# Kernel tuning notes

Measured on AMD Instinct MI355X. Metric: run time of the kernel, lower is better.

The kernel has to match this reference:

```python
import jax, jax.numpy as jnp
import numpy as np

EPS = 1e-3
MAX_ITER = 100
STAB = 1e-8


def setup_inputs() -> dict:
    key = jax.random.key(0)
    k1, k2 = jax.random.split(key)
    x = jax.random.normal(k1, (4, 4096, 8, 8), dtype=jnp.float32)
    y = jax.random.normal(k2, (4, 4096, 8, 8), dtype=jnp.float32)
    return {"x": x, "y": y}


def _sinkhorn_distance(x, y):
    B, N, H, W = x.shape
    d = H * W
    xf = jax.nn.softmax(x.reshape(B, N, d), axis=-1)  # [B,N,d]
    yf = jax.nn.softmax(y.reshape(B, N, d), axis=-1)  # [B,N,d]

    # squared euclidean distance: ||a-b||^2 = ||a||^2 + ||b||^2 - 2 a.b  (== cdist(p=2)**2)
    x2 = jnp.sum(xf * xf, axis=-1)  # [B,N]
    y2 = jnp.sum(yf * yf, axis=-1)  # [B,N]
    cross = jnp.einsum('bid,bjd->bij', xf, yf)  # [B,N,N]
    cost = jnp.maximum(x2[:, :, None] + y2[:, None, :] - 2.0 * cross, 0.0)

    K = jnp.exp(-cost / EPS)  # [B,N,N]

    u0 = jnp.full((B, N), 1.0 / N, dtype=x.dtype)
    v0 = jnp.full((B, N), 1.0 / N, dtype=x.dtype)

    def step(carry, _):
        u, v = carry
        u = 1.0 / (jnp.einsum('bij,bj->bi', K, v) + STAB)
        v = 1.0 / (jnp.einsum('bij,bi->bj', K, u) + STAB)
        return (u, v), None

    (u, v), _ = jax.lax.scan(step, (u0, v0), None, length=MAX_ITER)

    plan = u[:, :, None] * K * v[:, None, :]  # [B,N,N]
    dist = jnp.sum(plan * cost, axis=(1, 2))  # [B]
    return jnp.sum(dist)  # reduction='sum'


def reference(x, y):
    return _sinkhorn_distance(x, y)
```

## Files before the change

kernel.cpp:

```cpp
#include <hip/hip_runtime.h>
#include <stdint.h>

#define BB 4
#define NN 4096
#define DD 64
#define BN (BB*NN)
#define STABF 1e-8f
#define NITER 100
#define NEG_SCALE (-1442.695040888963f)

__device__ __forceinline__ float bf16lo(uint32_t w){ return __uint_as_float(w << 16); }
__device__ __forceinline__ float bf16hi(uint32_t w){ return __uint_as_float(w & 0xffff0000u); }
__device__ __forceinline__ uint32_t pack2bf(float f0, float f1){
  uint32_t u0 = __float_as_uint(f0); u0 += 0x7fffu + ((u0 >> 16) & 1u);
  uint32_t u1 = __float_as_uint(f1); u1 += 0x7fffu + ((u1 >> 16) & 1u);
  return (u0 >> 16) | (u1 & 0xffff0000u);
}

__global__ __launch_bounds__(256) void k_init(float* __restrict__ acc0,
                                              float* __restrict__ partial) {
  int idx = blockIdx.x * 256 + threadIdx.x;
  if (idx < BN) acc0[idx] = (float)NN;
  if (idx < 256) partial[idx] = 0.f;
}

__global__ __launch_bounds__(256) void k_softmax(
    const float* __restrict__ x, const float* __restrict__ y,
    float* __restrict__ xf, float* __restrict__ yf,
    float* __restrict__ x2, float* __restrict__ y2) {
  int wave = (blockIdx.x * 256 + threadIdx.x) >> 6;
  int lane = threadIdx.x & 63;
  const float* src; float* dst; float* d2; int row;
  if (wave < BN) { src = x; dst = xf; d2 = x2; row = wave; }
  else           { src = y; dst = yf; d2 = y2; row = wave - BN; }
  float v = src[(size_t)row * DD + lane];
  float m = v;
  #pragma unroll
  for (int off = 32; off; off >>= 1) m = fmaxf(m, __shfl_xor(m, off));
  float e = __expf(v - m);
  float s = e;
  #pragma unroll
  for (int off = 32; off; off >>= 1) s += __shfl_xor(s, off);
  float p = e / s;
  dst[(size_t)row * DD + lane] = p;
  float q = p * p;
  #pragma unroll
  for (int off = 32; off; off >>= 1) q += __shfl_xor(q, off);
  if (lane == 0) d2[row] = q;
}

__device__ __forceinline__ void fma_row(float av0, float av1, const float4 bv,
                                        float cr0[4], float cr1[4]) {
  cr0[0] = fmaf(av0, bv.x, cr0[0]); cr0[1] = fmaf(av0, bv.y, cr0[1]);
  cr0[2] = fmaf(av0, bv.z, cr0[2]); cr0[3] = fmaf(av0, bv.w, cr0[3]);
  cr1[0] = fmaf(av1, bv.x, cr1[0]); cr1[1] = fmaf(av1, bv.y, cr1[1]);
  cr1[2] = fmaf(av1, bv.z, cr1[2]); cr1[3] = fmaf(av1, bv.w, cr1[3]);
}

__global__ __launch_bounds__(256) void k_build(
    const float* __restrict__ xf, const float* __restrict__ yf,
    const float* __restrict__ x2, const float* __restrict__ y2,
    unsigned short* __restrict__ K) {
  __shared__ float sxf[32][68];
  __shared__ float syt[64][68];
  int bid = blockIdx.x, t = threadIdx.x;
  int jt = bid & 63, it = (bid >> 6) & 127, b = bid >> 13;
  int i0 = it * 32, j0 = jt * 64;
  {
    int r = t >> 3, c = (t & 7) * 8;
    const float* s0 = xf + ((size_t)(b*NN + i0 + r)) * DD + c;
    *(float4*)&sxf[r][c]     = *(const float4*)s0;
    *(float4*)&sxf[r][c + 4] = *(const float4*)(s0 + 4);
  }
  {
    int r = t >> 2, c0 = (t & 3) * 16;
    const float* s0 = yf + ((size_t)(b*NN + j0 + r)) * DD + c0;
    #pragma unroll
    for (int q = 0; q < 4; ++q) {
      float4 pv = *(const float4*)(s0 + q*4);
      syt[c0 + q*4 + 0][r] = pv.x;
      syt[c0 + q*4 + 1][r] = pv.y;
      syt[c0 + q*4 + 2][r] = pv.z;
      syt[c0 + q*4 + 3][r] = pv.w;
    }
  }
  __syncthreads();
  int tx = t & 15, ty = t >> 4;
  int ii = ty * 2, jj = tx * 4;
  float cr[2][4] = {{0,0,0,0},{0,0,0,0}};
  #pragma unroll
  for (int d = 0; d < DD; d += 4) {
    float4 a0 = *(const float4*)&sxf[ii][d];
    float4 a1 = *(const float4*)&sxf[ii + 1][d];
    float4 b0 = *(const float4*)&syt[d][jj];
    float4 b1 = *(const float4*)&syt[d + 1][jj];
    float4 b2 = *(const float4*)&syt[d + 2][jj];
    float4 b3 = *(const float4*)&syt[d + 3][jj];
    fma_row(a0.x, a1.x, b0, cr[0], cr[1]);
    fma_row(a0.y, a1.y, b1, cr[0], cr[1]);
    fma_row(a0.z, a1.z, b2, cr[0], cr[1]);
    fma_row(a0.w, a1.w, b3, cr[0], cr[1]);
  }
  float x2v[2], y2v[4];
  x2v[0] = x2[b*NN + i0 + ii]; x2v[1] = x2[b*NN + i0 + ii + 1];
  #pragma unroll
  for (int c = 0; c < 4; ++c) y2v[c] = y2[b*NN + j0 + jj + c];
  #pragma unroll
  for (int i2 = 0; i2 < 2; ++i2) {
    float k4[4];
    #pragma unroll
    for (int c = 0; c < 4; ++c) {
      float cost = fmaxf(x2v[i2] + y2v[c] - 2.f * cr[i2][c], 0.f);
      k4[c] = exp2f(cost * NEG_SCALE);
    }
    uint2 kw;
    kw.x = pack2bf(k4[0], k4[1]);
    kw.y = pack2bf(k4[2], k4[3]);
    *(uint2*)(K + ((size_t)(b*NN + i0 + ii + i2)) * NN + j0 + jj) = kw;
  }
}

__global__ __launch_bounds__(256) void k_rowdot(
    const unsigned short* __restrict__ K, const float* __restrict__ accIn,
    float* __restrict__ u, float* __restrict__ accZ) {
  int bid = blockIdx.x, t = threadIdx.x;
  if (bid < 16) {
    float4 z = make_float4(0.f, 0.f, 0.f, 0.f);
    *(float4*)(accZ + (size_t)(bid * 256 + t) * 4) = z;
  }
  int b = bid >> 8, g = bid & 255;
  int wave = t >> 6, lane = t & 63;
  const float* ap = accIn + (size_t)b * NN + lane * 8;
  float4 vr[16];
  #pragma unroll
  for (int c = 0; c < 8; ++c) {
    vr[2*c]   = *(const float4*)(ap + c * 512);
    vr[2*c+1] = *(const float4*)(ap + c * 512 + 4);
  }
  #pragma unroll
  for (int c = 0; c < 16; ++c) {
    vr[c].x = __builtin_amdgcn_rcpf(vr[c].x + STABF);
    vr[c].y = __builtin_amdgcn_rcpf(vr[c].y + STABF);
    vr[c].z = __builtin_amdgcn_rcpf(vr[c].z + STABF);
    vr[c].w = __builtin_amdgcn_rcpf(vr[c].w + STABF);
  }
  int row0 = g * 16 + wave * 4;
  const unsigned short* Kp = K + ((size_t)(b*NN + row0)) * NN + lane * 8;
  float s0 = 0.f, s1 = 0.f, s2 = 0.f, s3 = 0.f;
  #pragma unroll
  for (int c = 0; c < 8; ++c) {
    uint4 k0 = *(const uint4*)(Kp + (size_t)0 * NN + c * 512);
    uint4 k1 = *(const uint4*)(Kp + (size_t)1 * NN + c * 512);
    uint4 k2 = *(const uint4*)(Kp + (size_t)2 * NN + c * 512);
    uint4 k3 = *(const uint4*)(Kp + (size_t)3 * NN + c * 512);
    float4 a0 = vr[2*c], a1 = vr[2*c+1];
    s0 = fmaf(bf16lo(k0.x), a0.x, s0); s0 = fmaf(bf16hi(k0.x), a0.y, s0);
    s0 = fmaf(bf16lo(k0.y), a0.z, s0); s0 = fmaf(bf16hi(k0.y), a0.w, s0);
    s0 = fmaf(bf16lo(k0.z), a1.x, s0); s0 = fmaf(bf16hi(k0.z), a1.y, s0);
    s0 = fmaf(bf16lo(k0.w), a1.z, s0); s0 = fmaf(bf16hi(k0.w), a1.w, s0);
    s1 = fmaf(bf16lo(k1.x), a0.x, s1); s1 = fmaf(bf16hi(k1.x), a0.y, s1);
    s1 = fmaf(bf16lo(k1.y), a0.z, s1); s1 = fmaf(bf16hi(k1.y), a0.w, s1);
    s1 = fmaf(bf16lo(k1.z), a1.x, s1); s1 = fmaf(bf16hi(k1.z), a1.y, s1);
    s1 = fmaf(bf16lo(k1.w), a1.z, s1); s1 = fmaf(bf16hi(k1.w), a1.w, s1);
    s2 = fmaf(bf16lo(k2.x), a0.x, s2); s2 = fmaf(bf16hi(k2.x), a0.y, s2);
    s2 = fmaf(bf16lo(k2.y), a0.z, s2); s2 = fmaf(bf16hi(k2.y), a0.w, s2);
    s2 = fmaf(bf16lo(k2.z), a1.x, s2); s2 = fmaf(bf16hi(k2.z), a1.y, s2);
    s2 = fmaf(bf16lo(k2.w), a1.z, s2); s2 = fmaf(bf16hi(k2.w), a1.w, s2);
    s3 = fmaf(bf16lo(k3.x), a0.x, s3); s3 = fmaf(bf16hi(k3.x), a0.y, s3);
    s3 = fmaf(bf16lo(k3.y), a0.z, s3); s3 = fmaf(bf16hi(k3.y), a0.w, s3);
    s3 = fmaf(bf16lo(k3.z), a1.x, s3); s3 = fmaf(bf16hi(k3.z), a1.y, s3);
    s3 = fmaf(bf16lo(k3.w), a1.z, s3); s3 = fmaf(bf16hi(k3.w), a1.w, s3);
  }
  #pragma unroll
  for (int off = 32; off; off >>= 1) {
    s0 += __shfl_xor(s0, off);
    s1 += __shfl_xor(s1, off);
    s2 += __shfl_xor(s2, off);
    s3 += __shfl_xor(s3, off);
  }
  if (lane == 0) {
    float* up = u + b*NN + row0;
    up[0] = 1.0f / (s0 + STABF);
    up[1] = 1.0f / (s1 + STABF);
    up[2] = 1.0f / (s2 + STABF);
    up[3] = 1.0f / (s3 + STABF);
  }
}

__global__ __launch_bounds__(256) void k_coldot(
    const unsigned short* __restrict__ K, const float* __restrict__ u,
    float* __restrict__ acc) {
  int bid = blockIdx.x, t = threadIdx.x;
  int slab = bid & 1, chunk = (bid >> 1) & 63, b = bid >> 7;
  int i0 = chunk * 64;
  int j0 = slab * 2048 + t * 8;
  const unsigned short* Kp = K + ((size_t)(b*NN + i0)) * NN + j0;
  const float* up = u + b*NN + i0;
  float s0=0,s1=0,s2=0,s3=0,s4=0,s5=0,s6=0,s7=0;
  #pragma unroll 4
  for (int r = 0; r < 64; ++r) {
    uint4 kw = *(const uint4*)(Kp + (size_t)r * NN);
    float ur = up[r];
    s0 = fmaf(bf16lo(kw.x), ur, s0);
    s1 = fmaf(bf16hi(kw.x), ur, s1);
    s2 = fmaf(bf16lo(kw.y), ur, s2);
    s3 = fmaf(bf16hi(kw.y), ur, s3);
    s4 = fmaf(bf16lo(kw.z), ur, s4);
    s5 = fmaf(bf16hi(kw.z), ur, s5);
    s6 = fmaf(bf16lo(kw.w), ur, s6);
    s7 = fmaf(bf16hi(kw.w), ur, s7);
  }
  float* ap = acc + b*NN + j0;
  atomicAdd(ap + 0, s0); atomicAdd(ap + 1, s1);
  atomicAdd(ap + 2, s2); atomicAdd(ap + 3, s3);
  atomicAdd(ap + 4, s4); atomicAdd(ap + 5, s5);
  atomicAdd(ap + 6, s6); atomicAdd(ap + 7, s7);
}

__global__ __launch_bounds__(256) void k_final(
    const float* __restrict__ xf, const float* __restrict__ yf,
    const float* __restrict__ x2, const float* __restrict__ y2,
    const unsigned short* __restrict__ K, const float* __restrict__ u,
    const float* __restrict__ accv, float* __restrict__ partial) {
  __shared__ float sxf[32][68];
  __shared__ float syt[64][68];
  __shared__ float red[256];
  int bid = blockIdx.x, t = threadIdx.x;
  int jt = bid & 63, it = (bid >> 6) & 127, b = bid >> 13;
  int i0 = it * 32, j0 = jt * 64;
  {
    int r = t >> 3, c = (t & 7) * 8;
    const float* s0 = xf + ((size_t)(b*NN + i0 + r)) * DD + c;
    *(float4*)&sxf[r][c]     = *(const float4*)s0;
    *(float4*)&sxf[r][c + 4] = *(const float4*)(s0 + 4);
  }
  {
    int r = t >> 2, c0 = (t & 3) * 16;
    const float* s0 = yf + ((size_t)(b*NN + j0 + r)) * DD + c0;
    #pragma unroll
    for (int q = 0; q < 4; ++q) {
      float4 pv = *(const float4*)(s0 + q*4);
      syt[c0 + q*4 + 0][r] = pv.x;
      syt[c0 + q*4 + 1][r] = pv.y;
      syt[c0 + q*4 + 2][r] = pv.z;
      syt[c0 + q*4 + 3][r] = pv.w;
    }
  }
  __syncthreads();
  int tx = t & 15, ty = t >> 4;
  int ii = ty * 2, jj = tx * 4;
  float cr[2][4] = {{0,0,0,0},{0,0,0,0}};
  #pragma unroll
  for (int d = 0; d < DD; d += 4) {
    float4 a0 = *(const float4*)&sxf[ii][d];
    float4 a1 = *(const float4*)&sxf[ii + 1][d];
    float4 b0 = *(const float4*)&syt[d][jj];
    float4 b1 = *(const float4*)&syt[d + 1][jj];
    float4 b2 = *(const float4*)&syt[d + 2][jj];
    float4 b3 = *(const float4*)&syt[d + 3][jj];
    fma_row(a0.x, a1.x, b0, cr[0], cr[1]);
    fma_row(a0.y, a1.y, b1, cr[0], cr[1]);
    fma_row(a0.z, a1.z, b2, cr[0], cr[1]);
    fma_row(a0.w, a1.w, b3, cr[0], cr[1]);
  }
  float x2v[2], y2v[4], uv[2], vv[4];
  x2v[0] = x2[b*NN + i0 + ii]; x2v[1] = x2[b*NN + i0 + ii + 1];
  uv[0]  = u[b*NN + i0 + ii];  uv[1]  = u[b*NN + i0 + ii + 1];
  #pragma unroll
  for (int c = 0; c < 4; ++c) {
    y2v[c] = y2[b*NN + j0 + jj + c];
    vv[c]  = __builtin_amdgcn_rcpf(accv[b*NN + j0 + jj + c] + STABF);
  }
  float s = 0.f;
  #pragma unroll
  for (int i2 = 0; i2 < 2; ++i2) {
    uint2 kw = *(const uint2*)(K + ((size_t)(b*NN + i0 + ii + i2)) * NN + j0 + jj);
    float kk[4] = {bf16lo(kw.x), bf16hi(kw.x), bf16lo(kw.y), bf16hi(kw.y)};
    #pragma unroll
    for (int c = 0; c < 4; ++c) {
      float cost = fmaxf(x2v[i2] + y2v[c] - 2.f * cr[i2][c], 0.f);
      s = fmaf(uv[i2] * kk[c] * vv[c], cost, s);
    }
  }
  red[t] = s;
  __syncthreads();
  #pragma unroll
  for (int off = 128; off; off >>= 1) {
    if (t < off) red[t] += red[t + off];
    __syncthreads();
  }
  if (t == 0) atomicAdd(partial + (bid & 255), red[0]);
}

__global__ __launch_bounds__(256) void k_finalize(const float* __restrict__ partial,
                                                 float* __restrict__ out) {
  __shared__ float red[256];
  int t = threadIdx.x;
  red[t] = partial[t];
  __syncthreads();
  #pragma unroll
  for (int off = 128; off; off >>= 1) {
    if (t < off) red[t] += red[t + off];
    __syncthreads();
  }
  if (t == 0) out[0] = red[0];
}

extern "C" void kernel_launch(void* const* d_in, const int* in_sizes, int n_in,
                              void* d_out, int out_size, void* d_ws, size_t ws_size,
                              hipStream_t stream) {
  const float* x = (const float*)d_in[0];
  const float* y = (const float*)d_in[1];
  float* out = (float*)d_out;

  char* w = (char*)d_ws;
  unsigned short* K = (unsigned short*)w;
  float* xf = (float*)(w + (size_t)BN * NN * 2);
  float* yf = xf + (size_t)BN * DD;
  float* x2 = yf + (size_t)BN * DD;
  float* y2 = x2 + BN;
  float* uu = y2 + BN;
  float* acc = uu + BN;
  float* partial = acc + 2 * BN;
  (void)in_sizes; (void)n_in; (void)out_size; (void)ws_size;

  k_init<<<64, 256, 0, stream>>>(acc, partial);
  k_softmax<<<8192, 256, 0, stream>>>(x, y, xf, yf, x2, y2);
  k_build<<<32768, 256, 0, stream>>>(xf, yf, x2, y2, K);

  int p = 0;
  for (int itr = 0; itr < NITER; ++itr) {
    k_rowdot<<<1024, 256, 0, stream>>>(K, acc + (size_t)p * BN, uu, acc + (size_t)(1 - p) * BN);
    k_coldot<<<512, 256, 0, stream>>>(K, uu, acc + (size_t)(1 - p) * BN);
    p ^= 1;
  }
  k_final<<<32768, 256, 0, stream>>>(xf, yf, x2, y2, K, uu, acc, partial);
  k_finalize<<<1, 256, 0, stream>>>(partial, out);
}
```

Baseline: 7.698 ms.

## Fuse Sinkhorn row and column passes into one kernel with triple-buffered accumulators

```diff
diff --git a/kernel.cpp b/kernel.cpp
--- a/kernel.cpp
+++ b/kernel.cpp
@@ -18,9 +18,10 @@
 }
 
 __global__ __launch_bounds__(256) void k_init(float* __restrict__ acc0,
+                                              float* __restrict__ acc1,
                                               float* __restrict__ partial) {
   int idx = blockIdx.x * 256 + threadIdx.x;
-  if (idx < BN) acc0[idx] = (float)NN;
+  if (idx < BN) { acc0[idx] = (float)NN; acc1[idx] = 0.f; }
   if (idx < 256) partial[idx] = 0.f;
 }
 
@@ -120,101 +121,124 @@
   }
 }
 
-__global__ __launch_bounds__(256) void k_rowdot(
+__global__ __launch_bounds__(256, 2) void k_step(
     const unsigned short* __restrict__ K, const float* __restrict__ accIn,
-    float* __restrict__ u, float* __restrict__ accZ) {
+    float* __restrict__ accOut, float* __restrict__ accZero,
+    float* __restrict__ u) {
   int bid = blockIdx.x, t = threadIdx.x;
   if (bid < 16) {
     float4 z = make_float4(0.f, 0.f, 0.f, 0.f);
-    *(float4*)(accZ + (size_t)(bid * 256 + t) * 4) = z;
-  }
-  int b = bid >> 8, g = bid & 255;
+    *(float4*)(accZero + (size_t)(bid * 256 + t) * 4) = z;
+  }
+  int b = bid >> 7, chunk = bid & 127;
+  int i0 = chunk * 32;
   int wave = t >> 6, lane = t & 63;
-  const float* ap = accIn + (size_t)b * NN + lane * 8;
-  float4 vr[16];
-  #pragma unroll
-  for (int c = 0; c < 8; ++c) {
-    vr[2*c]   = *(const float4*)(ap + c * 512);
-    vr[2*c+1] = *(const float4*)(ap + c * 512 + 4);
-  }
-  #pragma unroll
-  for (int c = 0; c < 16; ++c) {
-    vr[c].x = __builtin_amdgcn_rcpf(vr[c].x + STABF);
-    vr[c].y = __builtin_amdgcn_rcpf(vr[c].y + STABF);
-    vr[c].z = __builtin_amdgcn_rcpf(vr[c].z + STABF);
-    vr[c].w = __builtin_amdgcn_rcpf(vr[c].w + STABF);
-  }
-  int row0 = g * 16 + wave * 4;
-  const unsigned short* Kp = K + ((size_t)(b*NN + row0)) * NN + lane * 8;
-  float s0 = 0.f, s1 = 0.f, s2 = 0.f, s3 = 0.f;
-  #pragma unroll
-  for (int c = 0; c < 8; ++c) {
-    uint4 k0 = *(const uint4*)(Kp + (size_t)0 * NN + c * 512);
-    uint4 k1 = *(const uint4*)(Kp + (size_t)1 * NN + c * 512);
-    uint4 k2 = *(const uint4*)(Kp + (size_t)2 * NN + c * 512);
-    uint4 k3 = *(const uint4*)(Kp + (size_t)3 * NN + c * 512);
-    float4 a0 = vr[2*c], a1 = vr[2*c+1];
-    s0 = fmaf(bf16lo(k0.x), a0.x, s0); s0 = fmaf(bf16hi(k0.x), a0.y, s0);
-    s0 = fmaf(bf16lo(k0.y), a0.z, s0); s0 = fmaf(bf16hi(k0.y), a0.w, s0);
-    s0 = fmaf(bf16lo(k0.z), a1.x, s0); s0 = fmaf(bf16hi(k0.z), a1.y, s0);
-    s0 = fmaf(bf16lo(k0.w), a1.z, s0); s0 = fmaf(bf16hi(k0.w), a1.w, s0);
-    s1 = fmaf(bf16lo(k1.x), a0.x, s1); s1 = fmaf(bf16hi(k1.x), a0.y, s1);
-    s1 = fmaf(bf16lo(k1.y), a0.z, s1); s1 = fmaf(bf16hi(k1.y), a0.w, s1);
-    s1 = fmaf(bf16lo(k1.z), a1.x, s1); s1 = fmaf(bf16hi(k1.z), a1.y, s1);
-    s1 = fmaf(bf16lo(k1.w), a1.z, s1); s1 = fmaf(bf16hi(k1.w), a1.w, s1);
-    s2 = fmaf(bf16lo(k2.x), a0.x, s2); s2 = fmaf(bf16hi(k2.x), a0.y, s2);
-    s2 = fmaf(bf16lo(k2.y), a0.z, s2); s2 = fmaf(bf16hi(k2.y), a0.w, s2);
-    s2 = fmaf(bf16lo(k2.z), a1.x, s2); s2 = fmaf(bf16hi(k2.z), a1.y, s2);
-    s2 = fmaf(bf16lo(k2.w), a1.z, s2); s2 = fmaf(bf16hi(k2.w), a1.w, s2);
-    s3 = fmaf(bf16lo(k3.x), a0.x, s3); s3 = fmaf(bf16hi(k3.x), a0.y, s3);
-    s3 = fmaf(bf16lo(k3.y), a0.z, s3); s3 = fmaf(bf16hi(k3.y), a0.w, s3);
-    s3 = fmaf(bf16lo(k3.z), a1.x, s3); s3 = fmaf(bf16hi(k3.z), a1.y, s3);
-    s3 = fmaf(bf16lo(k3.w), a1.z, s3); s3 = fmaf(bf16hi(k3.w), a1.w, s3);
-  }
-  #pragma unroll
-  for (int off = 32; off; off >>= 1) {
-    s0 += __shfl_xor(s0, off);
-    s1 += __shfl_xor(s1, off);
-    s2 += __shfl_xor(s2, off);
-    s3 += __shfl_xor(s3, off);
-  }
-  if (lane == 0) {
-    float* up = u + b*NN + row0;
-    up[0] = 1.0f / (s0 + STABF);
-    up[1] = 1.0f / (s1 + STABF);
-    up[2] = 1.0f / (s2 + STABF);
-    up[3] = 1.0f / (s3 + STABF);
-  }
-}
-
-__global__ __launch_bounds__(256) void k_coldot(
-    const unsigned short* __restrict__ K, const float* __restrict__ u,
-    float* __restrict__ acc) {
-  int bid = blockIdx.x, t = threadIdx.x;
-  int slab = bid & 1, chunk = (bid >> 1) & 63, b = bid >> 7;
-  int i0 = chunk * 64;
-  int j0 = slab * 2048 + t * 8;
-  const unsigned short* Kp = K + ((size_t)(b*NN + i0)) * NN + j0;
-  const float* up = u + b*NN + i0;
-  float s0=0,s1=0,s2=0,s3=0,s4=0,s5=0,s6=0,s7=0;
-  #pragma unroll 4
-  for (int r = 0; r < 64; ++r) {
-    uint4 kw = *(const uint4*)(Kp + (size_t)r * NN);
-    float ur = up[r];
-    s0 = fmaf(bf16lo(kw.x), ur, s0);
-    s1 = fmaf(bf16hi(kw.x), ur, s1);
-    s2 = fmaf(bf16lo(kw.y), ur, s2);
-    s3 = fmaf(bf16hi(kw.y), ur, s3);
-    s4 = fmaf(bf16lo(kw.z), ur, s4);
-    s5 = fmaf(bf16hi(kw.z), ur, s5);
-    s6 = fmaf(bf16lo(kw.w), ur, s6);
-    s7 = fmaf(bf16hi(kw.w), ur, s7);
-  }
-  float* ap = acc + b*NN + j0;
-  atomicAdd(ap + 0, s0); atomicAdd(ap + 1, s1);
-  atomicAdd(ap + 2, s2); atomicAdd(ap + 3, s3);
-  atomicAdd(ap + 4, s4); atomicAdd(ap + 5, s5);
-  atomicAdd(ap + 6, s6); atomicAdd(ap + 7, s7);
+  __shared__ float su[32];
+
+  {
+    const float* ap = accIn + (size_t)b * NN + lane * 8;
+    float4 vr[16];
+    #pragma unroll
+    for (int c = 0; c < 8; ++c) {
+      vr[2*c]   = *(const float4*)(ap + c * 512);
+      vr[2*c+1] = *(const float4*)(ap + c * 512 + 4);
+    }
+    #pragma unroll
+    for (int c = 0; c < 16; ++c) {
+      vr[c].x = __builtin_amdgcn_rcpf(vr[c].x + STABF);
+      vr[c].y = __builtin_amdgcn_rcpf(vr[c].y + STABF);
+      vr[c].z = __builtin_amdgcn_rcpf(vr[c].z + STABF);
+      vr[c].w = __builtin_amdgcn_rcpf(vr[c].w + STABF);
+    }
+    #pragma unroll
+    for (int grp = 0; grp < 2; ++grp) {
+      int lrow = wave * 8 + grp * 4;
+      int row0 = i0 + lrow;
+      const unsigned short* Kp = K + ((size_t)(b*NN + row0)) * NN + lane * 8;
+      float s0 = 0.f, s1 = 0.f, s2 = 0.f, s3 = 0.f;
+      #pragma unroll
+      for (int c = 0; c < 8; ++c) {
+        uint4 k0 = *(const uint4*)(Kp + (size_t)0 * NN + c * 512);
+        uint4 k1 = *(const uint4*)(Kp + (size_t)1 * NN + c * 512);
+        uint4 k2 = *(const uint4*)(Kp + (size_t)2 * NN + c * 512);
+        uint4 k3 = *(const uint4*)(Kp + (size_t)3 * NN + c * 512);
+        float4 a0 = vr[2*c], a1 = vr[2*c+1];
+        s0 = fmaf(bf16lo(k0.x), a0.x, s0); s0 = fmaf(bf16hi(k0.x), a0.y, s0);
+        s0 = fmaf(bf16lo(k0.y), a0.z, s0); s0 = fmaf(bf16hi(k0.y), a0.w, s0);
+        s0 = fmaf(bf16lo(k0.z), a1.x, s0); s0 = fmaf(bf16hi(k0.z), a1.y, s0);
+        s0 = fmaf(bf16lo(k0.w), a1.z, s0); s0 = fmaf(bf16hi(k0.w), a1.w, s0);
+        s1 = fmaf(bf16lo(k1.x), a0.x, s1); s1 = fmaf(bf16hi(k1.x), a0.y, s1);
+        s1 = fmaf(bf16lo(k1.y), a0.z, s1); s1 = fmaf(bf16hi(k1.y), a0.w, s1);
+        s1 = fmaf(bf16lo(k1.z), a1.x, s1); s1 = fmaf(bf16hi(k1.z), a1.y, s1);
+        s1 = fmaf(bf16lo(k1.w), a1.z, s1); s1 = fmaf(bf16hi(k1.w), a1.w, s1);
+        s2 = fmaf(bf16lo(k2.x), a0.x, s2); s2 = fmaf(bf16hi(k2.x), a0.y, s2);
+        s2 = fmaf(bf16lo(k2.y), a0.z, s2); s2 = fmaf(bf16hi(k2.y), a0.w, s2);
+        s2 = fmaf(bf16lo(k2.z), a1.x, s2); s2 = fmaf(bf16hi(k2.z), a1.y, s2);
+        s2 = fmaf(bf16lo(k2.w), a1.z, s2); s2 = fmaf(bf16hi(k2.w), a1.w, s2);
+        s3 = fmaf(bf16lo(k3.x), a0.x, s3); s3 = fmaf(bf16hi(k3.x), a0.y, s3);
+        s3 = fmaf(bf16lo(k3.y), a0.z, s3); s3 = fmaf(bf16hi(k3.y), a0.w, s3);
+        s3 = fmaf(bf16lo(k3.z), a1.x, s3); s3 = fmaf(bf16hi(k3.z), a1.y, s3);
+        s3 = fmaf(bf16lo(k3.w), a1.z, s3); s3 = fmaf(bf16hi(k3.w), a1.w, s3);
+      }
+      #pragma unroll
+      for (int off = 32; off; off >>= 1) {
+        s0 += __shfl_xor(s0, off);
+        s1 += __shfl_xor(s1, off);
+        s2 += __shfl_xor(s2, off);
+        s3 += __shfl_xor(s3, off);
+      }
+      if (lane == 0) {
+        float u0 = 1.0f / (s0 + STABF);
+        float u1 = 1.0f / (s1 + STABF);
+        float u2 = 1.0f / (s2 + STABF);
+        float u3 = 1.0f / (s3 + STABF);
+        su[lrow + 0] = u0; su[lrow + 1] = u1;
+        su[lrow + 2] = u2; su[lrow + 3] = u3;
+        float* up = u + b*NN + row0;
+        up[0] = u0; up[1] = u1; up[2] = u2; up[3] = u3;
+      }
+    }
+  }
+  __syncthreads();
+  {
+    int c0 = t * 8, c1 = 2048 + t * 8;
+    const unsigned short* Kp = K + ((size_t)(b*NN + i0)) * NN;
+    float s0=0,s1=0,s2=0,s3=0,s4=0,s5=0,s6=0,s7=0;
+    float q0=0,q1=0,q2=0,q3=0,q4=0,q5=0,q6=0,q7=0;
+    #pragma unroll 4
+    for (int r = 31; r >= 0; --r) {
+      const unsigned short* Kr = Kp + (size_t)r * NN;
+      uint4 ka = *(const uint4*)(Kr + c0);
+      uint4 kb = *(const uint4*)(Kr + c1);
+      float ur = su[r];
+      s0 = fmaf(bf16lo(ka.x), ur, s0);
+      s1 = fmaf(bf16hi(ka.x), ur, s1);
+      s2 = fmaf(bf16lo(ka.y), ur, s2);
+      s3 = fmaf(bf16hi(ka.y), ur, s3);
+      s4 = fmaf(bf16lo(ka.z), ur, s4);
+      s5 = fmaf(bf16hi(ka.z), ur, s5);
+      s6 = fmaf(bf16lo(ka.w), ur, s6);
+      s7 = fmaf(bf16hi(ka.w), ur, s7);
+      q0 = fmaf(bf16lo(kb.x), ur, q0);
+      q1 = fmaf(bf16hi(kb.x), ur, q1);
+      q2 = fmaf(bf16lo(kb.y), ur, q2);
+      q3 = fmaf(bf16hi(kb.y), ur, q3);
+      q4 = fmaf(bf16lo(kb.z), ur, q4);
+      q5 = fmaf(bf16hi(kb.z), ur, q5);
+      q6 = fmaf(bf16lo(kb.w), ur, q6);
+      q7 = fmaf(bf16hi(kb.w), ur, q7);
+    }
+    float* a0 = accOut + b*NN + c0;
+    atomicAdd(a0 + 0, s0); atomicAdd(a0 + 1, s1);
+    atomicAdd(a0 + 2, s2); atomicAdd(a0 + 3, s3);
+    atomicAdd(a0 + 4, s4); atomicAdd(a0 + 5, s5);
+    atomicAdd(a0 + 6, s6); atomicAdd(a0 + 7, s7);
+    float* a1 = accOut + b*NN + c1;
+    atomicAdd(a1 + 0, q0); atomicAdd(a1 + 1, q1);
+    atomicAdd(a1 + 2, q2); atomicAdd(a1 + 3, q3);
+    atomicAdd(a1 + 4, q4); atomicAdd(a1 + 5, q5);
+    atomicAdd(a1 + 6, q6); atomicAdd(a1 + 7, q7);
+  }
 }
 
 __global__ __launch_bounds__(256) void k_final(
@@ -320,20 +344,23 @@
   float* x2 = yf + (size_t)BN * DD;
   float* y2 = x2 + BN;
   float* uu = y2 + BN;
-  float* acc = uu + BN;
-  float* partial = acc + 2 * BN;
+  float* acc0 = uu + BN;
+  float* acc1 = acc0 + BN;
+  float* acc2 = acc1 + BN;
+  float* partial = acc2 + BN;
   (void)in_sizes; (void)n_in; (void)out_size; (void)ws_size;
 
-  k_init<<<64, 256, 0, stream>>>(acc, partial);
+  k_init<<<64, 256, 0, stream>>>(acc0, acc1, partial);
   k_softmax<<<8192, 256, 0, stream>>>(x, y, xf, yf, x2, y2);
   k_build<<<32768, 256, 0, stream>>>(xf, yf, x2, y2, K);
 
-  int p = 0;
-  for (int itr = 0; itr < NITER; ++itr) {
-    k_rowdot<<<1024, 256, 0, stream>>>(K, acc + (size_t)p * BN, uu, acc + (size_t)(1 - p) * BN);
-    k_coldot<<<512, 256, 0, stream>>>(K, uu, acc + (size_t)(1 - p) * BN);
-    p ^= 1;
-  }
-  k_final<<<32768, 256, 0, stream>>>(xf, yf, x2, y2, K, uu, acc, partial);
+  float* A[3] = {acc0, acc1, acc2};
+  for (int it = 0; it < NITER; ++it) {
+    float* aIn   = A[it % 3];
+    float* aOut  = A[(it + 1) % 3];
+    float* aZero = A[(it + 2) % 3];
+    k_step<<<512, 256, 0, stream>>>(K, aIn, aOut, aZero, uu);
+  }
+  k_final<<<32768, 256, 0, stream>>>(xf, yf, x2, y2, K, uu, A[1], partial);
   k_finalize<<<1, 256, 0, stream>>>(partial, out);
 }
```

Result: slower. 10.04 ms (+30.5%).
